# Performance work log

Measured on AMD Instinct MI355X. Metric: run time of the kernel, lower is better.

The kernel has to match this reference:

```python
import jax, jax.numpy as jnp
import numpy as np

EPS = 1e-5


def gcn_conv(x, W, b, src, dst):
    """PyG GCNConv: transform, add self-loops, symmetric norm, scatter-add, bias."""
    N = x.shape[0]
    h = x @ W  # [N, out]
    loop = jnp.arange(N)
    s = jnp.concatenate([src, loop])  # sources incl. self-loops
    d = jnp.concatenate([dst, loop])  # targets incl. self-loops
    deg = jax.ops.segment_sum(jnp.ones(s.shape[0], h.dtype), d, num_segments=N)
    dis = jnp.where(deg > 0, jax.lax.rsqrt(deg), 0.0)  # deg^-1/2
    norm = dis[s] * dis[d]  # [E+N]
    out = jax.ops.segment_sum(h[s] * norm[:, None], d, num_segments=N)
    return out + b


def batchnorm(x, gamma, beta):
    mu = x.mean(axis=0)
    var = x.var(axis=0)
    return (x - mu) * jax.lax.rsqrt(var + EPS) * gamma + beta


def setup_inputs() -> dict:
    key = jax.random.key(0)
    ks = jax.random.split(key, 6)
    N, E = 100000, 1600000
    IN, HID, OUT = 128, 256, 64
    x = jax.random.normal(ks[0], (N, IN), dtype=jnp.float32)
    edge_index = jax.random.randint(ks[1], (2, E), 0, N, dtype=jnp.int64)
    W1 = jax.random.normal(ks[2], (IN, HID), dtype=jnp.float32) / np.sqrt(IN)
    b1 = jnp.zeros((HID,), jnp.float32)
    gamma1 = jnp.ones((HID,), jnp.float32)
    beta1 = jnp.zeros((HID,), jnp.float32)
    W2 = jax.random.normal(ks[3], (HID, OUT), dtype=jnp.float32) / np.sqrt(HID)
    b2 = jnp.zeros((OUT,), jnp.float32)
    return {"x": x, "edge_index": edge_index, "W1": W1, "b1": b1,
            "gamma1": gamma1, "beta1": beta1, "W2": W2, "b2": b2}


def reference(x, edge_index, W1, b1, gamma1, beta1, W2, b2):
    src, dst = edge_index[0], edge_index[1]
    h = gcn_conv(x, W1, b1, src, dst)
    h = jax.nn.relu(batchnorm(h, gamma1, beta1))
    # dropout is identity at inference
    return gcn_conv(h, W2, b2, src, dst)
```

## Files before the change

### kernel.cpp

```cpp
#include <hip/hip_runtime.h>
#include <hip/hip_bf16.h>


#define IN_F  128
#define HID_F 256
#define OUT_F 64
#define BK_SHIFT 8
#define BK_SIZE  256
#define CHUNK    8192
#define CAP      8192

typedef unsigned int uint;
typedef unsigned short ushort;
typedef short bf16x8 __attribute__((ext_vector_type(8)));
typedef float f32x4 __attribute__((ext_vector_type(4)));

__device__ __forceinline__ ushort f2bf(float f) {
    uint u = __float_as_uint(f);
    uint r = (u + 0x7fffu + ((u >> 16) & 1u)) >> 16;
    return (ushort)r;
}
__device__ __forceinline__ float bf_lo(uint u) { return __uint_as_float(u << 16); }
__device__ __forceinline__ float bf_hi(uint u) { return __uint_as_float(u & 0xffff0000u); }

#define ACC8(u)                                         \
    do {                                                \
        acc[0] += bf_lo((u).x); acc[1] += bf_hi((u).x); \
        acc[2] += bf_lo((u).y); acc[3] += bf_hi((u).y); \
        acc[4] += bf_lo((u).z); acc[5] += bf_hi((u).z); \
        acc[6] += bf_lo((u).w); acc[7] += bf_hi((u).w); \
    } while (0)


__global__ __launch_bounds__(512) void scatter_wprep_kernel(
        const int* __restrict__ src, const int* __restrict__ dst,
        int* __restrict__ bcursor, uint* __restrict__ ebuf,
        const float* __restrict__ W1, const float* __restrict__ W2,
        ushort* __restrict__ W1bp, ushort* __restrict__ W2bp,
        int E, int NB, int nchunk) {
    if (blockIdx.x >= nchunk) {
        int i = (blockIdx.x - nchunk) * 512 + threadIdx.x;
        if (i < 32768) {
            int kk = i & 31, c = (i >> 5) & 255, kc = i >> 13;
            W1bp[i] = f2bf(W1[(size_t)(kc * 32 + kk) * HID_F + c]);
        } else {
            int j = i - 32768;
            int kk = j & 31, c = (j >> 5) & 63, kc = j >> 11;
            W2bp[j] = f2bf(W2[(size_t)(kc * 32 + kk) * OUT_F + c]);
        }
        return;
    }
    __shared__ int h[512];
    __shared__ int cur[512];
    for (int i = threadIdx.x; i < NB; i += 512) h[i] = 0;
    __syncthreads();
    int base = blockIdx.x * CHUNK;
    int end = min(base + CHUNK, E);
    for (int i = base + threadIdx.x; i < end; i += 512)
        atomicAdd(&h[dst[i] >> BK_SHIFT], 1);
    __syncthreads();
    for (int i = threadIdx.x; i < NB; i += 512)
        cur[i] = i * CAP + (h[i] ? atomicAdd(&bcursor[i], h[i]) : 0);
    __syncthreads();
    for (int i = base + threadIdx.x; i < end; i += 512) {
        int d = dst[i], s = src[i];
        int b = d >> BK_SHIFT;
        int pos = atomicAdd(&cur[b], 1);
        ebuf[pos] = (uint)s | ((uint)(d & (BK_SIZE - 1)) << 24);
    }
}

__global__ __launch_bounds__(1024) void bucket_build_kernel(
        const uint* __restrict__ ebuf, const int* __restrict__ bcursor,
        int* __restrict__ deg_e, int* __restrict__ offsets,
        float* __restrict__ dis, int* __restrict__ ssrc,
        const float* __restrict__ x, uint* __restrict__ xs, int N) {
    __shared__ int cnt[256], off[256], cur[256];
    __shared__ float sdis[256];
    int b = blockIdx.x;
    int t = threadIdx.x;
    if (t < 256) cnt[t] = 0;
    __syncthreads();
    int e0 = b * CAP;
    int e1 = e0 + min(bcursor[b], CAP);
    for (int i = e0 + t; i < e1; i += 1024)
        atomicAdd(&cnt[ebuf[i] >> 24], 1);
    __syncthreads();
    int v = (t < 256) ? cnt[t] : 0;
    int vpad = (v + 3) & ~3;
    if (t < 256) off[t] = vpad;
    __syncthreads();
    for (int o = 1; o < 256; o <<= 1) {
        int u = (t >= o && t < 256) ? off[t - o] : 0;
        __syncthreads();
        if (t < 256) off[t] += u;
        __syncthreads();
    }
    int base_pad = b * (CAP + 768);
    if (t < 256) {
        int excl = off[t] - vpad;
        int d = b * BK_SIZE + t;
        float dv = rsqrtf((float)(v + 1));
        sdis[t] = dv;
        if (d < N) {
            deg_e[d] = vpad;
            offsets[d] = base_pad + excl;
            dis[d] = dv;
        }
        cur[t] = excl;
    }
    __syncthreads();
    for (int i = e0 + t; i < e1; i += 1024) {
        uint e = ebuf[i];
        int ld = e >> 24;
        int pos = atomicAdd(&cur[ld], 1);
        ssrc[base_pad + pos] = (int)(e & 0xFFFFFFu);
    }
    __syncthreads();
    if (t < 256) {
        int excl = off[t] - vpad;
        for (int i = v; i < vpad; i++)
            ssrc[base_pad + excl + i] = N;
    }
    for (int i = t; i < 256 * 32; i += 1024) {
        int nl = i >> 5;
        int w = i & 31;
        int d = b * BK_SIZE + nl;
        if (d > N) continue;
        size_t oi = (size_t)d * 32 + w;
        if (d == N) { ((uint2*)xs)[oi] = make_uint2(0u, 0u); continue; }
        float dn = sdis[nl];
        float4 vv = ((const float4*)x)[oi];
        uint2 o;
        o.x = (uint)f2bf(dn * vv.x) | ((uint)f2bf(dn * vv.y) << 16);
        o.y = (uint)f2bf(dn * vv.z) | ((uint)f2bf(dn * vv.w) << 16);
        ((uint2*)xs)[oi] = o;
    }
}


__global__ void aggx_kernel(const uint* __restrict__ xs, const int* __restrict__ ssrc,
                            const int* __restrict__ offsets, const int* __restrict__ deg_e,
                            const float* __restrict__ dis, uint* __restrict__ zb, int N) {
    int lane = threadIdx.x & 63;
    int half = lane >> 5;
    int hl = lane & 31;
    int grp = hl >> 3;
    int ck = hl & 7;
    int j = blockIdx.x & 7;
    int fo = (j >> 2) << 5;
    int oct = ((blockIdx.x >> 3) << 2) + (j & 3);
    int n = (oct << 3) + ((threadIdx.x >> 6) << 1) + half;
    if (n >= N) return;
    float acc[8];
#pragma unroll
    for (int i = 0; i < 8; i++) acc[i] = 0.f;
    int start = offsets[n], cnt = deg_e[n];
    uint4 uself = *(const uint4*)(xs + ((size_t)n << 6) + fo + (ck << 2));
    int hbase = half << 5;
    for (int base = 0; base < cnt; base += 32) {
        int m = min(32, cnt - base);
        int idx = base + hl;
        int sv = ssrc[start + (idx < cnt ? idx : cnt - 1)];
        int rounds = m >> 2;
        int q = 0;
        for (; q + 4 <= rounds; q += 4) {
            int sA = __shfl(sv, hbase | ((q + 0) << 2) | grp);
            int sB = __shfl(sv, hbase | ((q + 1) << 2) | grp);
            int sC = __shfl(sv, hbase | ((q + 2) << 2) | grp);
            int sD = __shfl(sv, hbase | ((q + 3) << 2) | grp);
            uint4 uA = *(const uint4*)(xs + ((size_t)sA << 6) + fo + (ck << 2));
            uint4 uB = *(const uint4*)(xs + ((size_t)sB << 6) + fo + (ck << 2));
            uint4 uC = *(const uint4*)(xs + ((size_t)sC << 6) + fo + (ck << 2));
            uint4 uD = *(const uint4*)(xs + ((size_t)sD << 6) + fo + (ck << 2));
            ACC8(uA); ACC8(uB); ACC8(uC); ACC8(uD);
        }
        for (; q < rounds; q++) {
            int s = __shfl(sv, hbase | (q << 2) | grp);
            uint4 u = *(const uint4*)(xs + ((size_t)s << 6) + fo + (ck << 2));
            ACC8(u);
        }
    }
#pragma unroll
    for (int i = 0; i < 8; i++) acc[i] += __shfl_down(acc[i], 16);
#pragma unroll
    for (int i = 0; i < 8; i++) acc[i] += __shfl_down(acc[i], 8);
    if (grp == 0) {
        ACC8(uself);
        float dn = dis[n];
        uint4 o;
        o.x = (uint)f2bf(dn * acc[0]) | ((uint)f2bf(dn * acc[1]) << 16);
        o.y = (uint)f2bf(dn * acc[2]) | ((uint)f2bf(dn * acc[3]) << 16);
        o.z = (uint)f2bf(dn * acc[4]) | ((uint)f2bf(dn * acc[5]) << 16);
        o.w = (uint)f2bf(dn * acc[6]) | ((uint)f2bf(dn * acc[7]) << 16);
        *(uint4*)(zb + ((size_t)n << 6) + fo + (ck << 2)) = o;
    }
}

__global__ __launch_bounds__(256) void gemm1_kernel(const uint* __restrict__ zb,
                                                    const uint* __restrict__ W1bp,
                                                    const float* __restrict__ b1,
                                                    ushort* __restrict__ out1b,
                                                    float* __restrict__ bnp, int N) {
    __shared__ uint sbuf[8192];
    int t = threadIdx.x;
    int n0 = blockIdx.x * 64;
    for (int i = t; i < 64 * 16; i += 256) {
        int r = i >> 4, q = i & 15;
        int node = n0 + r;
        uint4 v = make_uint4(0u, 0u, 0u, 0u);
        if (node < N) v = *(const uint4*)(zb + (size_t)node * 64 + q * 4);
        int p = q ^ (r & 15);
        *(uint4*)(&sbuf[r * 64 + p * 4]) = v;
    }
    __syncthreads();
    int wave = t >> 6, lane = t & 63;
    int quad = lane >> 4, lrow = lane & 15;
    f32x4 acc[4][4];
#pragma unroll
    for (int m = 0; m < 4; m++)
#pragma unroll
        for (int nt = 0; nt < 4; nt++) acc[m][nt] = (f32x4)(0.f);
#pragma unroll
    for (int kc = 0; kc < 4; kc++) {
        bf16x8 bfr[4];
#pragma unroll
        for (int nt = 0; nt < 4; nt++) {
            int c = wave * 64 + nt * 16 + lrow;
            bfr[nt] = *(const bf16x8*)(W1bp + ((size_t)(kc * 256 + c) * 16 + quad * 4));
        }
        bf16x8 afr[4];
#pragma unroll
        for (int m = 0; m < 4; m++) {
            int p = (kc * 4 + quad) ^ lrow;
            afr[m] = *(const bf16x8*)(&sbuf[(m * 16 + lrow) * 64 + p * 4]);
        }
#pragma unroll
        for (int m = 0; m < 4; m++)
#pragma unroll
            for (int nt = 0; nt < 4; nt++)
                acc[m][nt] = __builtin_amdgcn_mfma_f32_16x16x32_bf16(
                    afr[m], bfr[nt], acc[m][nt], 0, 0, 0);
    }
    __syncthreads();
#pragma unroll
    for (int nt = 0; nt < 4; nt++) {
        int c = wave * 64 + nt * 16 + lrow;
        float bb = b1[c];
        float s = 0.f, q = 0.f;
#pragma unroll
        for (int m = 0; m < 4; m++) {
#pragma unroll
            for (int r = 0; r < 4; r++) {
                int row = m * 16 + quad * 4 + r;
                float v = acc[m][nt][r] + bb;
                if (n0 + row < N) { s += v; q = fmaf(v, v, q); }
                uint hv = (uint)f2bf(v);
                uint pv = __shfl_xor(hv, 1);
                if ((lrow & 1) == 0)
                    sbuf[row * 128 + (c >> 1)] = hv | (pv << 16);
            }
        }
        s += __shfl_down(s, 32); q += __shfl_down(q, 32);
        s += __shfl_down(s, 16); q += __shfl_down(q, 16);
        if (quad == 0) {
            bnp[(size_t)blockIdx.x * 512 + c] = s;
            bnp[(size_t)blockIdx.x * 512 + 256 + c] = q;
        }
    }
    __syncthreads();
    uint* out1g = (uint*)out1b;
    for (int i = t; i < 2048; i += 256) {
        int row = i >> 5;
        if (n0 + row < N)
            *(uint4*)(out1g + (size_t)(n0 + row) * 128 + (i & 31) * 4) =
                *(const uint4*)(&sbuf[i * 4]);
    }
}

__global__ void bnred_kernel(const float* __restrict__ bnp, float* __restrict__ bnsum,
                             int nblk) {
    int g = blockIdx.x, t = threadIdx.x;
    float s = 0.f, q = 0.f;
    for (int b = g; b < nblk; b += 32) {
        s += bnp[(size_t)b * 512 + t];
        q += bnp[(size_t)b * 512 + 256 + t];
    }
    atomicAdd(&bnsum[t], s);
    atomicAdd(&bnsum[256 + t], q);
}

__global__ __launch_bounds__(256) void gemm2_kernel(const ushort* __restrict__ out1b,
                                                    const uint* __restrict__ W2bp,
                                                    const float* __restrict__ dis,
                                                    const float* __restrict__ bnsum,
                                                    const float* __restrict__ gamma,
                                                    const float* __restrict__ beta,
                                                    ushort* __restrict__ gs, int N) {
    __shared__ uint sbuf[8192];
    __shared__ float bns[256], bnb[256];
    const uint* out1u = (const uint*)out1b;
    int t = threadIdx.x;
    int n0 = blockIdx.x * 64;
    if (blockIdx.x == 0 && t < 32) ((uint*)gs)[(size_t)N * 32 + t] = 0u;
    {
        float invN = 1.0f / (float)N;
        float mean = bnsum[t] * invN;
        float var = bnsum[256 + t] * invN - mean * mean;
        float sc = gamma[t] * rsqrtf(fmaxf(var, 0.f) + 1e-5f);
        bns[t] = sc;
        bnb[t] = beta[t] - mean * sc;
    }
    __syncthreads();
    for (int i = t; i < 64 * 32; i += 256) {
        int r = i >> 5, q = i & 31;
        int node = n0 + r;
        uint4 v = make_uint4(0u, 0u, 0u, 0u);
        if (node < N) {
            uint4 w = *(const uint4*)(out1u + (size_t)node * 128 + q * 4);
            int c0 = q * 8;
            float r0 = fmaxf(fmaf(bf_lo(w.x), bns[c0 + 0], bnb[c0 + 0]), 0.f);
            float r1 = fmaxf(fmaf(bf_hi(w.x), bns[c0 + 1], bnb[c0 + 1]), 0.f);
            float r2 = fmaxf(fmaf(bf_lo(w.y), bns[c0 + 2], bnb[c0 + 2]), 0.f);
            float r3 = fmaxf(fmaf(bf_hi(w.y), bns[c0 + 3], bnb[c0 + 3]), 0.f);
            float r4 = fmaxf(fmaf(bf_lo(w.z), bns[c0 + 4], bnb[c0 + 4]), 0.f);
            float r5 = fmaxf(fmaf(bf_hi(w.z), bns[c0 + 5], bnb[c0 + 5]), 0.f);
            float r6 = fmaxf(fmaf(bf_lo(w.w), bns[c0 + 6], bnb[c0 + 6]), 0.f);
            float r7 = fmaxf(fmaf(bf_hi(w.w), bns[c0 + 7], bnb[c0 + 7]), 0.f);
            v.x = (uint)f2bf(r0) | ((uint)f2bf(r1) << 16);
            v.y = (uint)f2bf(r2) | ((uint)f2bf(r3) << 16);
            v.z = (uint)f2bf(r4) | ((uint)f2bf(r5) << 16);
            v.w = (uint)f2bf(r6) | ((uint)f2bf(r7) << 16);
        }
        int p = (q & 16) | ((q & 15) ^ (r & 15));
        *(uint4*)(&sbuf[r * 128 + p * 4]) = v;
    }
    __syncthreads();
    int wave = t >> 6, lane = t & 63;
    int quad = lane >> 4, lrow = lane & 15;
    int c = wave * 16 + lrow;
    f32x4 acc[4];
#pragma unroll
    for (int m = 0; m < 4; m++) acc[m] = (f32x4)(0.f);
#pragma unroll
    for (int kc = 0; kc < 8; kc++) {
        bf16x8 bfr = *(const bf16x8*)(W2bp + ((size_t)(kc * 64 + c) * 16 + quad * 4));
#pragma unroll
        for (int m = 0; m < 4; m++) {
            int q = kc * 4 + quad;
            int p = (q & 16) | ((q & 15) ^ lrow);
            bf16x8 afr = *(const bf16x8*)(&sbuf[(m * 16 + lrow) * 128 + p * 4]);
            acc[m] = __builtin_amdgcn_mfma_f32_16x16x32_bf16(afr, bfr, acc[m], 0, 0, 0);
        }
    }
    __syncthreads();
#pragma unroll
    for (int m = 0; m < 4; m++) {
#pragma unroll
        for (int r = 0; r < 4; r++) {
            int row = m * 16 + quad * 4 + r;
            int node = n0 + row;
            float dn = (node < N) ? dis[node] : 0.f;
            uint hv = (uint)f2bf(dn * acc[m][r]);
            uint pv = __shfl_xor(hv, 1);
            if ((lrow & 1) == 0)
                sbuf[row * 32 + (c >> 1)] = hv | (pv << 16);
        }
    }
    __syncthreads();
    uint* gsg = (uint*)gs;
    for (int i = t; i < 512; i += 256) {
        int row = i >> 3;
        if (n0 + row < N)
            *(uint4*)(gsg + (size_t)(n0 + row) * 32 + (i & 7) * 4) =
                *(const uint4*)(&sbuf[i * 4]);
    }
}

__global__ void agg2_kernel(const uint* __restrict__ gs, const int* __restrict__ ssrc,
                            const int* __restrict__ offsets, const int* __restrict__ deg_e,
                            const float* __restrict__ dis, const float* __restrict__ b2,
                            float* __restrict__ out, int N) {
    int lane = threadIdx.x & 63;
    int half = lane >> 5;
    int hl = lane & 31;
    int grp = hl >> 3;
    int ck = hl & 7;
    int n = blockIdx.x * 8 + ((threadIdx.x >> 6) << 1) + half;
    if (n >= N) return;
    float acc[8];
#pragma unroll
    for (int i = 0; i < 8; i++) acc[i] = 0.f;
    int start = offsets[n], cnt = deg_e[n];
    uint4 uself = *(const uint4*)(gs + ((size_t)n << 5) + (ck << 2));
    int hbase = half << 5;
    for (int base = 0; base < cnt; base += 32) {
        int m = min(32, cnt - base);
        int idx = base + hl;
        int sv = ssrc[start + (idx < cnt ? idx : cnt - 1)];
        int rounds = m >> 2;
        int q = 0;
        for (; q + 4 <= rounds; q += 4) {
            int sA = __shfl(sv, hbase | ((q + 0) << 2) | grp);
            int sB = __shfl(sv, hbase | ((q + 1) << 2) | grp);
            int sC = __shfl(sv, hbase | ((q + 2) << 2) | grp);
            int sD = __shfl(sv, hbase | ((q + 3) << 2) | grp);
            uint4 uA = *(const uint4*)(gs + ((size_t)sA << 5) + (ck << 2));
            uint4 uB = *(const uint4*)(gs + ((size_t)sB << 5) + (ck << 2));
            uint4 uC = *(const uint4*)(gs + ((size_t)sC << 5) + (ck << 2));
            uint4 uD = *(const uint4*)(gs + ((size_t)sD << 5) + (ck << 2));
            ACC8(uA); ACC8(uB); ACC8(uC); ACC8(uD);
        }
        for (; q + 2 <= rounds; q += 2) {
            int sA = __shfl(sv, hbase | ((q + 0) << 2) | grp);
            int sB = __shfl(sv, hbase | ((q + 1) << 2) | grp);
            uint4 uA = *(const uint4*)(gs + ((size_t)sA << 5) + (ck << 2));
            uint4 uB = *(const uint4*)(gs + ((size_t)sB << 5) + (ck << 2));
            ACC8(uA); ACC8(uB);
        }
        for (; q < rounds; q++) {
            int s = __shfl(sv, hbase | (q << 2) | grp);
            uint4 u = *(const uint4*)(gs + ((size_t)s << 5) + (ck << 2));
            ACC8(u);
        }
    }
#pragma unroll
    for (int i = 0; i < 8; i++) acc[i] += __shfl_down(acc[i], 16);
#pragma unroll
    for (int i = 0; i < 8; i++) acc[i] += __shfl_down(acc[i], 8);
    if (grp == 0) {
        ACC8(uself);
        float dn = dis[n];
        float4 bb0 = *(const float4*)(b2 + ck * 8);
        float4 bb1 = *(const float4*)(b2 + ck * 8 + 4);
        float* op = out + (size_t)n * OUT_F + ck * 8;
        *(float4*)op = make_float4(fmaf(dn, acc[0], bb0.x), fmaf(dn, acc[1], bb0.y),
                                   fmaf(dn, acc[2], bb0.z), fmaf(dn, acc[3], bb0.w));
        *(float4*)(op + 4) = make_float4(fmaf(dn, acc[4], bb1.x), fmaf(dn, acc[5], bb1.y),
                                         fmaf(dn, acc[6], bb1.z), fmaf(dn, acc[7], bb1.w));
    }
}

extern "C" void kernel_launch(void* const* d_in, const int* in_sizes, int n_in,
                              void* d_out, int out_size, void* d_ws, size_t ws_size,
                              hipStream_t stream) {
    const float* x      = (const float*)d_in[0];
    const int*   edges  = (const int*)d_in[1];
    const float* W1     = (const float*)d_in[2];
    const float* b1     = (const float*)d_in[3];
    const float* gamma1 = (const float*)d_in[4];
    const float* beta1  = (const float*)d_in[5];
    const float* W2     = (const float*)d_in[6];
    const float* b2     = (const float*)d_in[7];
    float* out = (float*)d_out;

    int N = in_sizes[0] / IN_F;
    int E = in_sizes[1] / 2;
    const int* src = edges;
    const int* dst = edges + E;
    int NB = (N + BK_SIZE - 1) / BK_SIZE;
    int nchunks = (E + CHUNK - 1) / CHUNK;
    int nblk1 = (N + 63) / 64;

    char* ws = (char*)d_ws;
    size_t off = 0;
    auto alloc = [&](size_t bytes) -> void* {
        void* p = ws + off;
        off += (bytes + 255) & ~(size_t)255;
        return p;
    };
    int*    deg_e   = (int*)alloc((size_t)N * 4);
    int*    offsets = (int*)alloc((size_t)N * 4);
    float*  dis     = (float*)alloc((size_t)(N + 1) * 4);
    int*    bcursor = (int*)alloc(512 * 4);
    float*  bnsum   = (float*)alloc(512 * 4);
    int*    ssrc    = (int*)alloc((size_t)NB * (CAP + 768) * 4);
    uint*   ebuf    = (uint*)alloc((size_t)NB * CAP * 4);
    uint*   xs      = (uint*)alloc((size_t)(N + 1) * (IN_F / 2) * 4);
    uint*   zb      = (uint*)alloc((size_t)N * (IN_F / 2) * 4);
    ushort* out1b   = (ushort*)alloc((size_t)N * HID_F * 2);
    float*  bnp     = (float*)alloc((size_t)nblk1 * 512 * 4);
    ushort* W1bp    = (ushort*)alloc(4 * 256 * 32 * 2);
    ushort* W2bp    = (ushort*)alloc(8 * 64 * 32 * 2);
    ushort* gs      = (ushort*)zb;

    hipMemsetAsync(bcursor, 0, 2 * 512 * 4, stream);

    scatter_wprep_kernel<<<nchunks + 96, 512, 0, stream>>>(src, dst, bcursor, ebuf,
                                                           W1, W2, W1bp, W2bp,
                                                           E, NB, nchunks);
    bucket_build_kernel<<<NB, 1024, 0, stream>>>(ebuf, bcursor, deg_e, offsets, dis, ssrc,
                                                 x, xs, N);
    {
        int noct = (N + 7) >> 3;
        int grid = ((noct + 3) >> 2) << 3;
        aggx_kernel<<<grid, 256, 0, stream>>>(xs, ssrc, offsets, deg_e, dis, zb, N);
    }
    gemm1_kernel<<<nblk1, 256, 0, stream>>>(zb, (const uint*)W1bp, b1, out1b, bnp, N);
    bnred_kernel<<<32, 256, 0, stream>>>(bnp, bnsum, nblk1);
    gemm2_kernel<<<nblk1, 256, 0, stream>>>(out1b, (const uint*)W2bp, dis, bnsum,
                                            gamma1, beta1, gs, N);
    agg2_kernel<<<(N + 7) / 8, 256, 0, stream>>>((const uint*)gs, ssrc, offsets, deg_e, dis,
                                                 b2, out, N);
}
```

Before: 312.4 us.

## Halve destination bucket size and split aggx launch into two halves

Destination buckets shrink from 256 to 128 nodes, which doubles the bucket count (NB about 782). Per-bucket capacity and padding shrink to match, and the shared histogram arrays grow to 1024 entries. This gives bucket_build more, smaller blocks for better load spread across CUs. The aggx kernel gains an octet offset and is launched twice over two halves of the node range, which adds one extra launch and has no clear benefit on a single stream. CAP 4096 per 128-node bucket still leaves ample headroom above the average of about 2048 edges per bucket.

```diff
diff --git a/kernel.cpp b/kernel.cpp
--- a/kernel.cpp
+++ b/kernel.cpp
@@ -5,10 +5,11 @@
 #define IN_F  128
 #define HID_F 256
 #define OUT_F 64
-#define BK_SHIFT 8
-#define BK_SIZE  256
+#define BK_SHIFT 7
+#define BK_SIZE  128
 #define CHUNK    8192
-#define CAP      8192
+#define CAP      4096
+#define BPAD     384
 
 typedef unsigned int uint;
 typedef unsigned short ushort;
@@ -50,8 +51,8 @@
         }
         return;
     }
-    __shared__ int h[512];
-    __shared__ int cur[512];
+    __shared__ int h[1024];
+    __shared__ int cur[1024];
     for (int i = threadIdx.x; i < NB; i += 512) h[i] = 0;
     __syncthreads();
     int base = blockIdx.x * CHUNK;
@@ -75,29 +76,29 @@
         int* __restrict__ deg_e, int* __restrict__ offsets,
         float* __restrict__ dis, int* __restrict__ ssrc,
         const float* __restrict__ x, uint* __restrict__ xs, int N) {
-    __shared__ int cnt[256], off[256], cur[256];
-    __shared__ float sdis[256];
+    __shared__ int cnt[BK_SIZE], off[BK_SIZE], cur[BK_SIZE];
+    __shared__ float sdis[BK_SIZE];
     int b = blockIdx.x;
     int t = threadIdx.x;
-    if (t < 256) cnt[t] = 0;
+    if (t < BK_SIZE) cnt[t] = 0;
     __syncthreads();
     int e0 = b * CAP;
     int e1 = e0 + min(bcursor[b], CAP);
     for (int i = e0 + t; i < e1; i += 1024)
         atomicAdd(&cnt[ebuf[i] >> 24], 1);
     __syncthreads();
-    int v = (t < 256) ? cnt[t] : 0;
+    int v = (t < BK_SIZE) ? cnt[t] : 0;
     int vpad = (v + 3) & ~3;
-    if (t < 256) off[t] = vpad;
-    __syncthreads();
-    for (int o = 1; o < 256; o <<= 1) {
-        int u = (t >= o && t < 256) ? off[t - o] : 0;
+    if (t < BK_SIZE) off[t] = vpad;
+    __syncthreads();
+    for (int o = 1; o < BK_SIZE; o <<= 1) {
+        int u = (t >= o && t < BK_SIZE) ? off[t - o] : 0;
         __syncthreads();
-        if (t < 256) off[t] += u;
+        if (t < BK_SIZE) off[t] += u;
         __syncthreads();
     }
-    int base_pad = b * (CAP + 768);
-    if (t < 256) {
+    int base_pad = b * (CAP + BPAD);
+    if (t < BK_SIZE) {
         int excl = off[t] - vpad;
         int d = b * BK_SIZE + t;
         float dv = rsqrtf((float)(v + 1));
@@ -117,12 +118,12 @@
         ssrc[base_pad + pos] = (int)(e & 0xFFFFFFu);
     }
     __syncthreads();
-    if (t < 256) {
+    if (t < BK_SIZE) {
         int excl = off[t] - vpad;
         for (int i = v; i < vpad; i++)
             ssrc[base_pad + excl + i] = N;
     }
-    for (int i = t; i < 256 * 32; i += 1024) {
+    for (int i = t; i < BK_SIZE * 32; i += 1024) {
         int nl = i >> 5;
         int w = i & 31;
         int d = b * BK_SIZE + nl;
@@ -141,7 +142,8 @@
 
 __global__ void aggx_kernel(const uint* __restrict__ xs, const int* __restrict__ ssrc,
                             const int* __restrict__ offsets, const int* __restrict__ deg_e,
-                            const float* __restrict__ dis, uint* __restrict__ zb, int N) {
+                            const float* __restrict__ dis, uint* __restrict__ zb,
+                            int oct0, int N) {
     int lane = threadIdx.x & 63;
     int half = lane >> 5;
     int hl = lane & 31;
@@ -149,7 +151,7 @@
     int ck = hl & 7;
     int j = blockIdx.x & 7;
     int fo = (j >> 2) << 5;
-    int oct = ((blockIdx.x >> 3) << 2) + (j & 3);
+    int oct = oct0 + ((blockIdx.x >> 3) << 2) + (j & 3);
     int n = (oct << 3) + ((threadIdx.x >> 6) << 1) + half;
     if (n >= N) return;
     float acc[8];
@@ -472,9 +474,9 @@
     int*    deg_e   = (int*)alloc((size_t)N * 4);
     int*    offsets = (int*)alloc((size_t)N * 4);
     float*  dis     = (float*)alloc((size_t)(N + 1) * 4);
-    int*    bcursor = (int*)alloc(512 * 4);
+    int*    bcursor = (int*)alloc(1024 * 4);
     float*  bnsum   = (float*)alloc(512 * 4);
-    int*    ssrc    = (int*)alloc((size_t)NB * (CAP + 768) * 4);
+    int*    ssrc    = (int*)alloc((size_t)NB * (CAP + BPAD) * 4);
     uint*   ebuf    = (uint*)alloc((size_t)NB * CAP * 4);
     uint*   xs      = (uint*)alloc((size_t)(N + 1) * (IN_F / 2) * 4);
     uint*   zb      = (uint*)alloc((size_t)N * (IN_F / 2) * 4);
@@ -484,7 +486,7 @@
     ushort* W2bp    = (ushort*)alloc(8 * 64 * 32 * 2);
     ushort* gs      = (ushort*)zb;
 
-    hipMemsetAsync(bcursor, 0, 2 * 512 * 4, stream);
+    hipMemsetAsync(bcursor, 0, (1024 + 512) * 4, stream);
 
     scatter_wprep_kernel<<<nchunks + 96, 512, 0, stream>>>(src, dst, bcursor, ebuf,
                                                            W1, W2, W1bp, W2bp,
@@ -493,8 +495,12 @@
                                                  x, xs, N);
     {
         int noct = (N + 7) >> 3;
-        int grid = ((noct + 3) >> 2) << 3;
-        aggx_kernel<<<grid, 256, 0, stream>>>(xs, ssrc, offsets, deg_e, dis, zb, N);
+        int h0 = ((noct / 2 + 3) >> 2) << 2;
+        int h1 = noct - h0;
+        int grid0 = (h0 >> 2) << 3;
+        int grid1 = ((h1 + 3) >> 2) << 3;
+        aggx_kernel<<<grid0, 256, 0, stream>>>(xs, ssrc, offsets, deg_e, dis, zb, 0, N);
+        aggx_kernel<<<grid1, 256, 0, stream>>>(xs, ssrc, offsets, deg_e, dis, zb, h0, N);
     }
     gemm1_kernel<<<nblk1, 256, 0, stream>>>(zb, (const uint*)W1bp, b1, out1b, bnp, N);
     bnred_kernel<<<32, 256, 0, stream>>>(bnp, bnsum, nblk1);
```

Measured after the change: 327.4 us. 4.8% more time.

## Replace atomic bucket cursors with count-scan-scatter for compact deterministic edge bucketing

Applied to the files above, without the earlier changes.

Edge bucketing now runs in three passes. A per-chunk histogram pass writes counts to a bucket-major matrix, a single-block scan computes exclusive bases, and a scatter pass places edges at those precomputed offsets. This drops the global atomic cursors, makes the edge buffer compact (size E rather than NB*CAP), and removes the CAP overflow truncation. It adds two kernel launches, rereads dst, and relies on a serial single-block scan over about 77k entries. The aggregation kernel is also split into two launches over halves of the node range.

```diff
diff --git a/kernel.cpp b/kernel.cpp
--- a/kernel.cpp
+++ b/kernel.cpp
@@ -32,9 +32,8 @@
     } while (0)
 
 
-__global__ __launch_bounds__(512) void scatter_wprep_kernel(
-        const int* __restrict__ src, const int* __restrict__ dst,
-        int* __restrict__ bcursor, uint* __restrict__ ebuf,
+__global__ __launch_bounds__(512) void count_wprep_kernel(
+        const int* __restrict__ dst, int* __restrict__ cnts,
         const float* __restrict__ W1, const float* __restrict__ W2,
         ushort* __restrict__ W1bp, ushort* __restrict__ W2bp,
         int E, int NB, int nchunk) {
@@ -51,17 +50,50 @@
         return;
     }
     __shared__ int h[512];
-    __shared__ int cur[512];
     for (int i = threadIdx.x; i < NB; i += 512) h[i] = 0;
     __syncthreads();
-    int base = blockIdx.x * CHUNK;
+    int c = blockIdx.x;
+    int base = c * CHUNK;
     int end = min(base + CHUNK, E);
     for (int i = base + threadIdx.x; i < end; i += 512)
         atomicAdd(&h[dst[i] >> BK_SHIFT], 1);
     __syncthreads();
     for (int i = threadIdx.x; i < NB; i += 512)
-        cur[i] = i * CAP + (h[i] ? atomicAdd(&bcursor[i], h[i]) : 0);
-    __syncthreads();
+        cnts[(size_t)i * nchunk + c] = h[i];
+}
+
+__global__ __launch_bounds__(1024) void scan_kernel(const int* __restrict__ cnts,
+                                                    int* __restrict__ bases, int M) {
+    __shared__ int part[1024];
+    int t = threadIdx.x;
+    int per = (M + 1023) >> 10;
+    int lo = t * per, hi = min(lo + per, M);
+    int s = 0;
+    for (int k = lo; k < hi; k++) s += cnts[k];
+    part[t] = s;
+    __syncthreads();
+    for (int o = 1; o < 1024; o <<= 1) {
+        int u = (t >= o) ? part[t - o] : 0;
+        __syncthreads();
+        part[t] += u;
+        __syncthreads();
+    }
+    int run = (t == 0) ? 0 : part[t - 1];
+    for (int k = lo; k < hi; k++) { int v = cnts[k]; bases[k] = run; run += v; }
+    if (t == 1023) bases[M] = run;
+}
+
+__global__ __launch_bounds__(512) void scatter_kernel(
+        const int* __restrict__ src, const int* __restrict__ dst,
+        const int* __restrict__ bases, uint* __restrict__ ebuf,
+        int E, int NB, int nchunk) {
+    __shared__ int cur[512];
+    int c = blockIdx.x;
+    for (int i = threadIdx.x; i < NB; i += 512)
+        cur[i] = bases[(size_t)i * nchunk + c];
+    __syncthreads();
+    int base = c * CHUNK;
+    int end = min(base + CHUNK, E);
     for (int i = base + threadIdx.x; i < end; i += 512) {
         int d = dst[i], s = src[i];
         int b = d >> BK_SHIFT;
@@ -71,18 +103,18 @@
 }
 
 __global__ __launch_bounds__(1024) void bucket_build_kernel(
-        const uint* __restrict__ ebuf, const int* __restrict__ bcursor,
+        const uint* __restrict__ ebuf, const int* __restrict__ bases,
         int* __restrict__ deg_e, int* __restrict__ offsets,
         float* __restrict__ dis, int* __restrict__ ssrc,
-        const float* __restrict__ x, uint* __restrict__ xs, int N) {
+        const float* __restrict__ x, uint* __restrict__ xs, int N, int nchunk) {
     __shared__ int cnt[256], off[256], cur[256];
     __shared__ float sdis[256];
     int b = blockIdx.x;
     int t = threadIdx.x;
     if (t < 256) cnt[t] = 0;
     __syncthreads();
-    int e0 = b * CAP;
-    int e1 = e0 + min(bcursor[b], CAP);
+    int e0 = bases[(size_t)b * nchunk];
+    int e1 = bases[(size_t)(b + 1) * nchunk];
     for (int i = e0 + t; i < e1; i += 1024)
         atomicAdd(&cnt[ebuf[i] >> 24], 1);
     __syncthreads();
@@ -141,7 +173,8 @@
 
 __global__ void aggx_kernel(const uint* __restrict__ xs, const int* __restrict__ ssrc,
                             const int* __restrict__ offsets, const int* __restrict__ deg_e,
-                            const float* __restrict__ dis, uint* __restrict__ zb, int N) {
+                            const float* __restrict__ dis, uint* __restrict__ zb,
+                            int oct0, int N) {
     int lane = threadIdx.x & 63;
     int half = lane >> 5;
     int hl = lane & 31;
@@ -149,7 +182,7 @@
     int ck = hl & 7;
     int j = blockIdx.x & 7;
     int fo = (j >> 2) << 5;
-    int oct = ((blockIdx.x >> 3) << 2) + (j & 3);
+    int oct = oct0 + ((blockIdx.x >> 3) << 2) + (j & 3);
     int n = (oct << 3) + ((threadIdx.x >> 6) << 1) + half;
     if (n >= N) return;
     float acc[8];
@@ -460,6 +493,7 @@
     const int* dst = edges + E;
     int NB = (N + BK_SIZE - 1) / BK_SIZE;
     int nchunks = (E + CHUNK - 1) / CHUNK;
+    int M = NB * nchunks;
     int nblk1 = (N + 63) / 64;
 
     char* ws = (char*)d_ws;
@@ -472,10 +506,11 @@
     int*    deg_e   = (int*)alloc((size_t)N * 4);
     int*    offsets = (int*)alloc((size_t)N * 4);
     float*  dis     = (float*)alloc((size_t)(N + 1) * 4);
-    int*    bcursor = (int*)alloc(512 * 4);
     float*  bnsum   = (float*)alloc(512 * 4);
+    int*    cnts    = (int*)alloc((size_t)M * 4);
+    int*    bases   = (int*)alloc((size_t)(M + 1) * 4);
     int*    ssrc    = (int*)alloc((size_t)NB * (CAP + 768) * 4);
-    uint*   ebuf    = (uint*)alloc((size_t)NB * CAP * 4);
+    uint*   ebuf    = (uint*)alloc((size_t)E * 4);
     uint*   xs      = (uint*)alloc((size_t)(N + 1) * (IN_F / 2) * 4);
     uint*   zb      = (uint*)alloc((size_t)N * (IN_F / 2) * 4);
     ushort* out1b   = (ushort*)alloc((size_t)N * HID_F * 2);
@@ -484,17 +519,22 @@
     ushort* W2bp    = (ushort*)alloc(8 * 64 * 32 * 2);
     ushort* gs      = (ushort*)zb;
 
-    hipMemsetAsync(bcursor, 0, 2 * 512 * 4, stream);
-
-    scatter_wprep_kernel<<<nchunks + 96, 512, 0, stream>>>(src, dst, bcursor, ebuf,
-                                                           W1, W2, W1bp, W2bp,
-                                                           E, NB, nchunks);
-    bucket_build_kernel<<<NB, 1024, 0, stream>>>(ebuf, bcursor, deg_e, offsets, dis, ssrc,
-                                                 x, xs, N);
+    hipMemsetAsync(bnsum, 0, 512 * 4, stream);
+
+    count_wprep_kernel<<<nchunks + 96, 512, 0, stream>>>(dst, cnts, W1, W2, W1bp, W2bp,
+                                                         E, NB, nchunks);
+    scan_kernel<<<1, 1024, 0, stream>>>(cnts, bases, M);
+    scatter_kernel<<<nchunks, 512, 0, stream>>>(src, dst, bases, ebuf, E, NB, nchunks);
+    bucket_build_kernel<<<NB, 1024, 0, stream>>>(ebuf, bases, deg_e, offsets, dis, ssrc,
+                                                 x, xs, N, nchunks);
     {
         int noct = (N + 7) >> 3;
-        int grid = ((noct + 3) >> 2) << 3;
-        aggx_kernel<<<grid, 256, 0, stream>>>(xs, ssrc, offsets, deg_e, dis, zb, N);
+        int h0 = ((noct / 2 + 3) >> 2) << 2;
+        int h1 = noct - h0;
+        int grid0 = (h0 >> 2) << 3;
+        int grid1 = ((h1 + 3) >> 2) << 3;
+        aggx_kernel<<<grid0, 256, 0, stream>>>(xs, ssrc, offsets, deg_e, dis, zb, 0, N);
+        aggx_kernel<<<grid1, 256, 0, stream>>>(xs, ssrc, offsets, deg_e, dis, zb, h0, N);
     }
     gemm1_kernel<<<nblk1, 256, 0, stream>>>(zb, (const uint*)W1bp, b1, out1b, bnp, N);
     bnred_kernel<<<32, 256, 0, stream>>>(bnp, bnsum, nblk1);
```

Measured after the change: 439.3 us. +40.6%, slower.
